# Kernel optimization log

Measured on AMD Instinct MI355X. Metric: run time of the kernel, lower is better.

The kernel has to match this reference:

```python
import jax, jax.numpy as jnp
import numpy as np

B, F, D, H = 16384, 10, 512, 8
DH = D // H
EPS = 1e-5


def setup_inputs() -> dict:
    key = jax.random.key(0)
    ks = jax.random.split(key, 12)
    s = 1.0 / np.sqrt(D)
    inp = {
        "x": jax.random.normal(ks[0], (B, F), dtype=jnp.float32),
        # per-feature Linear(1, D): weight (F, D), bias (F, D)
        "Wf": jax.random.normal(ks[1], (F, D), dtype=jnp.float32) * 1.0,
        "bf": jax.random.normal(ks[2], (F, D), dtype=jnp.float32) * 0.1,
        # MHA in/out projections (torch layout: out_features x in_features)
        "Wq": jax.random.normal(ks[3], (D, D), dtype=jnp.float32) * s,
        "Wk": jax.random.normal(ks[4], (D, D), dtype=jnp.float32) * s,
        "Wv": jax.random.normal(ks[5], (D, D), dtype=jnp.float32) * s,
        "bq": jax.random.normal(ks[6], (D,), dtype=jnp.float32) * 0.02,
        "bk": jax.random.normal(ks[7], (D,), dtype=jnp.float32) * 0.02,
        "bv": jax.random.normal(ks[8], (D,), dtype=jnp.float32) * 0.02,
        "Wo": jax.random.normal(ks[9], (D, D), dtype=jnp.float32) * s,
        "bo": jax.random.normal(ks[10], (D,), dtype=jnp.float32) * 0.02,
        "gamma": jnp.ones((D,), dtype=jnp.float32),
        "beta": jnp.zeros((D,), dtype=jnp.float32),
    }
    return inp


def reference(x, Wf, bf, Wq, Wk, Wv, bq, bk, bv, Wo, bo, gamma, beta):
    # Fused per-feature scalar Linear + ReLU: (B,F,1)*(F,D) + (F,D) -> (B,F,D)
    p = jax.nn.relu(x[:, :, None] * Wf[None] + bf[None])
    # Multi-head self-attention (q = k = v = p), torch Linear: y = x @ W.T + b
    def heads(t):  # (B,F,D) -> (B,H,F,DH)
        return t.reshape(B, F, H, DH).transpose(0, 2, 1, 3)
    q = heads(p @ Wq.T + bq)
    k = heads(p @ Wk.T + bk)
    v = heads(p @ Wv.T + bv)
    scores = jnp.einsum("bhqd,bhkd->bhqk", q, k) / jnp.sqrt(jnp.float32(DH))
    attn = jax.nn.softmax(scores, axis=-1)
    o = jnp.einsum("bhqk,bhkd->bhqd", attn, v)
    o = o.transpose(0, 2, 1, 3).reshape(B, F, D) @ Wo.T + bo
    # LayerNorm over last dim
    mu = jnp.mean(o, axis=-1, keepdims=True)
    var = jnp.mean(jnp.square(o - mu), axis=-1, keepdims=True)
    ln = (o - mu) * jax.lax.rsqrt(var + EPS) * gamma + beta
    # sum pool over the function/sequence axis
    return jnp.sum(ln, axis=1)  # (B, D)
```

## Files before the change

### kernel.cpp

```cpp
#include <hip/hip_runtime.h>
#include <stdint.h>


typedef __bf16 bf16;
typedef __bf16 bf16x8 __attribute__((ext_vector_type(8)));
typedef float f32x4 __attribute__((ext_vector_type(4)));

#define EPS 1e-5f

static constexpr size_t O_ELEMS   = (size_t)16384 * 10 * 512;
static constexpr size_t O_BYTES   = O_ELEMS * 2;
static constexpr size_t WQKV_ELEMS = (size_t)8 * 192 * 512;
static constexpr size_t WQKV_BYTES = WQKV_ELEMS * 2;

__device__ __forceinline__ void async_copy16(void* lds, const void* g) {
  __builtin_amdgcn_global_load_lds(
      (const __attribute__((address_space(1))) uint32_t*)g,
      (__attribute__((address_space(3))) uint32_t*)lds, 16, 0, 0);
}

__global__ __launch_bounds__(256) void pack_weights(
    const float* __restrict__ Wq, const float* __restrict__ Wk,
    const float* __restrict__ Wv, const float* __restrict__ Wo,
    bf16* __restrict__ wqkv, bf16* __restrict__ wob) {
  int idx = blockIdx.x * 256 + threadIdx.x;
#pragma unroll
  for (int u = 0; u < 4; ++u) {
    int i = idx + u * 262144;
    if (i < 786432) {
      int pr = i >> 9, k = i & 511;
      int h = pr / 192, w = pr - h * 192;
      int t = w >> 6, r = w & 63;
      const float* src = (t == 0) ? Wq : ((t == 1) ? Wk : Wv);
      wqkv[i] = (bf16)src[(h * 64 + r) * 512 + k];
    } else {
      int j = i - 786432;
      wob[j] = (bf16)Wo[j];
    }
  }
}

__global__ __launch_bounds__(512, 2) void kern_attn(
    const float* __restrict__ x, const float* __restrict__ Wf,
    const float* __restrict__ bfv, const bf16* __restrict__ wqkv,
    const float* __restrict__ bq, const float* __restrict__ bk,
    const float* __restrict__ bv, bf16* __restrict__ O) {
  __shared__ __align__(16) char sA[8 * 80 * 128];
  __shared__ __align__(16) char sB0[24576];
  __shared__ __align__(16) char sB1[24576];
  __shared__ __align__(16) char sQK[88 * 256];

  bf16* vbuf = (bf16*)sB1;
  float* scp = (float*)(sB1 + 10240);

  const int tid = threadIdx.x;
  const int wave = tid >> 6;
  const int lane = tid & 63;
  const int lm = lane & 15;
  const int lg = lane >> 4;
  const int wm = wave >> 2;
  const int wn = wave & 3;
  const int b0 = blockIdx.x * 8;
  const int lr = lane >> 3;
  const int kcp2 = lane & 7;
  const int kcg = kcp2 ^ lr;

#pragma unroll
  for (int jb = 0; jb < 3; ++jb) {
    int rb = wave + 8 * jb;
    async_copy16(sB0 + rb * 1024, wqkv + (size_t)(rb * 8 + lr) * 512 + kcg * 8);
  }

#pragma unroll
  for (int it = 0; it < 10; ++it) {
    int c = tid + it * 512;
    int s = c / 640, rem = c - s * 640;
    int r = rem >> 3, kcp = rem & 7;
    int kc = kcp ^ (r & 7);
    int k = s * 64 + kc * 8;
    int bl = r / 10, f = r - bl * 10;
    float xv = x[(b0 + bl) * 10 + f];
    const float* wf = Wf + f * 512 + k;
    const float* bp = bfv + f * 512 + k;
    bf16x8 pv;
#pragma unroll
    for (int j = 0; j < 8; ++j) pv[j] = (bf16)fmaxf(xv * wf[j] + bp[j], 0.f);
    *(bf16x8*)(sA + s * 10240 + r * 128 + kcp * 16) = pv;
  }
  __syncthreads();

  const int x7 = lm & 7;

  for (int h = 0; h < 8; ++h) {
    f32x4 acc[3][3];
#pragma unroll
    for (int i = 0; i < 3; ++i)
#pragma unroll
      for (int j = 0; j < 3; ++j) { f32x4 z = {0.f, 0.f, 0.f, 0.f}; acc[i][j] = z; }

    for (int s = 0; s < 8; ++s) {
      int t = h * 8 + s;
      char* bufC = (s & 1) ? sB1 : sB0;
      char* bufN = (s & 1) ? sB0 : sB1;
      if (t != 63) {
        int tn = t + 1;
        int h2 = tn >> 3, s2 = tn & 7;
        const bf16* srcb = wqkv + (size_t)h2 * 98304 + s2 * 64 + kcg * 8;
#pragma unroll
        for (int jb = 0; jb < 3; ++jb) {
          int rb = wave + 8 * jb;
          async_copy16(bufN + rb * 1024, srcb + (size_t)(rb * 8 + lr) * 512);
        }
      }
#pragma unroll
      for (int kk = 0; kk < 2; ++kk) {
        int kcl = kk * 4 + lg;
        int ch = (kcl ^ x7) << 4;
        bf16x8 af[3], bfr[3];
#pragma unroll
        for (int mt = 0; mt < 3; ++mt) {
          int m = wm * 48 + mt * 16 + lm;
          af[mt] = *(const bf16x8*)(sA + s * 10240 + m * 128 + ch);
        }
#pragma unroll
        for (int nt = 0; nt < 3; ++nt) {
          int n = wn * 48 + nt * 16 + lm;
          bfr[nt] = *(const bf16x8*)(bufC + n * 128 + ch);
        }
#pragma unroll
        for (int mt = 0; mt < 3; ++mt)
#pragma unroll
          for (int nt = 0; nt < 3; ++nt)
            acc[mt][nt] = __builtin_amdgcn_mfma_f32_16x16x32_bf16(af[mt], bfr[nt], acc[mt][nt], 0, 0, 0);
      }
      __syncthreads();
    }

    {
      float bias[3];
#pragma unroll
      for (int nt = 0; nt < 3; ++nt) {
        int col = wn * 48 + nt * 16 + lm;
        bias[nt] = (col < 64) ? bq[h * 64 + col]
                 : (col < 128) ? bk[h * 64 + col - 64]
                 : bv[h * 64 + col - 128];
      }
#pragma unroll
      for (int mt = 0; mt < 3; ++mt) {
        int rowb = wm * 48 + mt * 16 + lg * 4;
        if (rowb < 80) {
#pragma unroll
          for (int r = 0; r < 4; ++r) {
            int rw = rowb + r;
#pragma unroll
            for (int nt = 0; nt < 3; ++nt) {
              int col = wn * 48 + nt * 16 + lm;
              float val = acc[mt][nt][r] + bias[nt];
              if (col < 128)
                *(bf16*)(sQK + rw * 256 + (((col >> 3) ^ (rw & 7)) << 4) + (col & 7) * 2) = (bf16)val;
              else
                vbuf[rw * 64 + (col - 128)] = (bf16)val;
            }
          }
        }
      }
    }
    __syncthreads();

    {
      const int b = wave;
      f32x4 sv = {0.f, 0.f, 0.f, 0.f};
      const int rowa = b * 10 + lm;
      const int x7r = rowa & 7;
#pragma unroll
      for (int kk = 0; kk < 2; ++kk) {
        bf16x8 qf = *(const bf16x8*)(sQK + rowa * 256 + (((kk * 4 + lg) ^ x7r) << 4));
        bf16x8 kf = *(const bf16x8*)(sQK + rowa * 256 + (((8 + kk * 4 + lg) ^ x7r) << 4));
        sv = __builtin_amdgcn_mfma_f32_16x16x32_bf16(qf, kf, sv, 0, 0, 0);
      }
#pragma unroll
      for (int r = 0; r < 4; ++r) {
        float val = (lm < 10) ? sv[r] * 0.125f : -1e30f;
        float mx = val;
#pragma unroll
        for (int off = 1; off < 16; off <<= 1) mx = fmaxf(mx, __shfl_xor(mx, off));
        float e = __expf(val - mx);
        float ssum = e;
#pragma unroll
        for (int off = 1; off < 16; off <<= 1) ssum += __shfl_xor(ssum, off);
        int i = lg * 4 + r;
        if (i < 10 && lm < 12) scp[(b * 10 + i) * 12 + lm] = e / ssum;
      }
    }

    {
      const int b = wave;
      const int d = lane;
      float vv[10];
#pragma unroll
      for (int j = 0; j < 10; ++j) vv[j] = (float)vbuf[(b * 10 + j) * 64 + d];
      bf16* Ob = O + ((size_t)(b0 + b) * 10) * 512 + h * 64 + d;
#pragma unroll
      for (int i = 0; i < 10; ++i) {
        const float* ar = scp + (b * 10 + i) * 12;
        f32x4 a0 = *(const f32x4*)ar;
        f32x4 a1 = *(const f32x4*)(ar + 4);
        float o = a0[0] * vv[0] + a0[1] * vv[1] + a0[2] * vv[2] + a0[3] * vv[3]
                + a1[0] * vv[4] + a1[1] * vv[5] + a1[2] * vv[6] + a1[3] * vv[7]
                + ar[8] * vv[8] + ar[9] * vv[9];
        Ob[(size_t)i * 512] = (bf16)o;
      }
    }
    __syncthreads();
  }
}

__global__ __launch_bounds__(256, 2) void kern_out(
    const bf16* __restrict__ O, const bf16* __restrict__ wob,
    const float* __restrict__ bo, const float* __restrict__ gamma,
    const float* __restrict__ beta, float* __restrict__ out) {
  __shared__ __align__(16) char sAB[71680];
  __shared__ float partial[48][4][2];
  __shared__ float stats[48][2];
  char* As = sAB;
  char* Bs = sAB + 6144;
  bf16* lnb = (bf16*)sAB;

  const int tid = threadIdx.x;
  const int wave = tid >> 6, lane = tid & 63;
  const int lm = lane & 15, lg = lane >> 4;
  const int m0 = blockIdx.x * 40;

  f32x4 acc[3][8];
#pragma unroll
  for (int i = 0; i < 3; ++i)
#pragma unroll
    for (int j = 0; j < 8; ++j) { f32x4 z = {0.f, 0.f, 0.f, 0.f}; acc[i][j] = z; }

  const int lr = lane >> 3;
  const int kcp2 = lane & 7;
  const int kcg = kcp2 ^ lr;

  for (int s = 0; s < 8; ++s) {
    {
      int rr = wave * 8 + lr;
      int rm = min(rr, 39);
      async_copy16(As + wave * 1024, O + (size_t)(m0 + rm) * 512 + s * 64 + kcg * 8);
      if (wave < 2) {
        int rr2 = (4 + wave) * 8 + lr;
        int rm2 = min(rr2, 39);
        async_copy16(As + (4 + wave) * 1024, O + (size_t)(m0 + rm2) * 512 + s * 64 + kcg * 8);
      }
    }
#pragma unroll
    for (int jb = 0; jb < 16; ++jb) {
      int rb = wave + 4 * jb;
      int n = rb * 8 + lr;
      async_copy16(Bs + rb * 1024, wob + (size_t)n * 512 + s * 64 + kcg * 8);
    }
    __syncthreads();
#pragma unroll
    for (int kk = 0; kk < 2; ++kk) {
      int kcl = kk * 4 + lg;
      bf16x8 af[3], bfr[8];
#pragma unroll
      for (int mt = 0; mt < 3; ++mt) {
        int m = mt * 16 + lm;
        af[mt] = *(const bf16x8*)(As + m * 128 + ((kcl ^ (m & 7)) << 4));
      }
#pragma unroll
      for (int nt = 0; nt < 8; ++nt) {
        int n = wave * 128 + nt * 16 + lm;
        bfr[nt] = *(const bf16x8*)(Bs + n * 128 + ((kcl ^ (n & 7)) << 4));
      }
#pragma unroll
      for (int mt = 0; mt < 3; ++mt)
#pragma unroll
        for (int nt = 0; nt < 8; ++nt)
          acc[mt][nt] = __builtin_amdgcn_mfma_f32_16x16x32_bf16(af[mt], bfr[nt], acc[mt][nt], 0, 0, 0);
    }
    __syncthreads();
  }

#pragma unroll
  for (int nt = 0; nt < 8; ++nt) {
    int col = wave * 128 + nt * 16 + lm;
    float bb = bo[col];
#pragma unroll
    for (int mt = 0; mt < 3; ++mt)
#pragma unroll
      for (int r = 0; r < 4; ++r) acc[mt][nt][r] += bb;
  }

#pragma unroll
  for (int mt = 0; mt < 3; ++mt)
#pragma unroll
    for (int r = 0; r < 4; ++r) {
      float s1 = 0.f, s2 = 0.f;
#pragma unroll
      for (int nt = 0; nt < 8; ++nt) { float v = acc[mt][nt][r]; s1 += v; s2 += v * v; }
#pragma unroll
      for (int off = 1; off < 16; off <<= 1) {
        s1 += __shfl_xor(s1, off);
        s2 += __shfl_xor(s2, off);
      }
      if (lm == 0) {
        int row = mt * 16 + lg * 4 + r;
        partial[row][wave][0] = s1;
        partial[row][wave][1] = s2;
      }
    }
  __syncthreads();
  if (tid < 48) {
    float s1 = partial[tid][0][0] + partial[tid][1][0] + partial[tid][2][0] + partial[tid][3][0];
    float s2 = partial[tid][0][1] + partial[tid][1][1] + partial[tid][2][1] + partial[tid][3][1];
    float mu = s1 * (1.f / 512.f);
    float var = s2 * (1.f / 512.f) - mu * mu;
    stats[tid][0] = mu;
    stats[tid][1] = rsqrtf(var + EPS);
  }
  __syncthreads();
#pragma unroll
  for (int mt = 0; mt < 3; ++mt)
#pragma unroll
    for (int r = 0; r < 4; ++r) {
      int row = mt * 16 + lg * 4 + r;
      float mu = stats[row][0], rr = stats[row][1];
#pragma unroll
      for (int nt = 0; nt < 8; ++nt) {
        int col = wave * 128 + nt * 16 + lm;
        lnb[row * 520 + col] = (bf16)((acc[mt][nt][r] - mu) * rr);
      }
    }
  __syncthreads();
#pragma unroll
  for (int u = 0; u < 8; ++u) {
    int id = tid + u * 256;
    int b = id >> 9, n = id & 511;
    float ssum = 0.f;
#pragma unroll
    for (int f = 0; f < 10; ++f) ssum += (float)lnb[(b * 10 + f) * 520 + n];
    out[(size_t)(blockIdx.x * 4 + b) * 512 + n] = gamma[n] * ssum + 10.f * beta[n];
  }
}

extern "C" void kernel_launch(void* const* d_in, const int* in_sizes, int n_in,
                              void* d_out, int out_size, void* d_ws, size_t ws_size,
                              hipStream_t stream) {
  const float* x     = (const float*)d_in[0];
  const float* Wf    = (const float*)d_in[1];
  const float* bfv   = (const float*)d_in[2];
  const float* Wq    = (const float*)d_in[3];
  const float* Wk    = (const float*)d_in[4];
  const float* Wv    = (const float*)d_in[5];
  const float* bq    = (const float*)d_in[6];
  const float* bk    = (const float*)d_in[7];
  const float* bv    = (const float*)d_in[8];
  const float* Wo    = (const float*)d_in[9];
  const float* bo    = (const float*)d_in[10];
  const float* gamma = (const float*)d_in[11];
  const float* beta  = (const float*)d_in[12];
  float* out = (float*)d_out;

  char* ws = (char*)d_ws;
  bf16* O    = (bf16*)ws;
  bf16* wqkv = (bf16*)(ws + O_BYTES);
  bf16* wob  = (bf16*)(ws + O_BYTES + WQKV_BYTES);

  pack_weights<<<1024, 256, 0, stream>>>(Wq, Wk, Wv, Wo, wqkv, wob);
  kern_attn<<<2048, 512, 0, stream>>>(x, Wf, bfv, wqkv, bq, bk, bv, O);
  kern_out<<<4096, 256, 0, stream>>>(O, wob, bo, gamma, beta, out);
}
```

Baseline: 790.4 us.

## Fuse output projection and LayerNorm pooling into attention kernel

Merges the attention kernel and the output-projection/LayerNorm/sum-pool kernel into one launch, so each block processes its 80 rows through Wo right after computing attention. The O intermediate is still written to global memory, but it is read back by the same block, likely from L2, which avoids the separate launch and its 40-row tiling. The change also prefetches the A fragments for the next k-step into registers, skips the padded third m-tile for the upper waves, and raises MFMA wave priority with s_setprio. In exchange, LDS use grows to about 150KB per block, which may lower occupancy from the intended 2 blocks per CU.

```diff
diff --git a/kernel.cpp b/kernel.cpp
--- a/kernel.cpp
+++ b/kernel.cpp
@@ -10,8 +10,7 @@
 
 static constexpr size_t O_ELEMS   = (size_t)16384 * 10 * 512;
 static constexpr size_t O_BYTES   = O_ELEMS * 2;
-static constexpr size_t WQKV_ELEMS = (size_t)8 * 192 * 512;
-static constexpr size_t WQKV_BYTES = WQKV_ELEMS * 2;
+static constexpr size_t WQKV_BYTES = (size_t)8 * 192 * 512 * 2;
 
 __device__ __forceinline__ void async_copy16(void* lds, const void* g) {
   __builtin_amdgcn_global_load_lds(
@@ -40,16 +39,19 @@
   }
 }
 
-__global__ __launch_bounds__(512, 2) void kern_attn(
+__global__ __launch_bounds__(512, 2) void kern_fused(
     const float* __restrict__ x, const float* __restrict__ Wf,
     const float* __restrict__ bfv, const bf16* __restrict__ wqkv,
     const float* __restrict__ bq, const float* __restrict__ bk,
-    const float* __restrict__ bv, bf16* __restrict__ O) {
-  __shared__ __align__(16) char sA[8 * 80 * 128];
-  __shared__ __align__(16) char sB0[24576];
-  __shared__ __align__(16) char sB1[24576];
-  __shared__ __align__(16) char sQK[88 * 256];
-
+    const float* __restrict__ bv, bf16* __restrict__ O,
+    const bf16* __restrict__ wob, const float* __restrict__ bo,
+    const float* __restrict__ gamma, const float* __restrict__ beta,
+    float* __restrict__ out) {
+  __shared__ __align__(16) char smem[153600];
+  char* sA  = smem;
+  char* sB0 = smem + 81920;
+  char* sB1 = smem + 106496;
+  char* sQK = smem + 131072;
   bf16* vbuf = (bf16*)sB1;
   float* scp = (float*)(sB1 + 10240);
 
@@ -62,8 +64,8 @@
   const int wn = wave & 3;
   const int b0 = blockIdx.x * 8;
   const int lr = lane >> 3;
-  const int kcp2 = lane & 7;
-  const int kcg = kcp2 ^ lr;
+  const int kcg = (lane & 7) ^ lr;
+  const int x7 = lm & 7;
 
 #pragma unroll
   for (int jb = 0; jb < 3; ++jb) {
@@ -89,7 +91,15 @@
   }
   __syncthreads();
 
-  const int x7 = lm & 7;
+  bf16x8 af[2][3];
+#pragma unroll
+  for (int kk = 0; kk < 2; ++kk)
+#pragma unroll
+    for (int mt = 0; mt < 3; ++mt)
+      if (mt < 2 || wm == 0) {
+        int m = wm * 48 + mt * 16 + lm;
+        af[kk][mt] = *(const bf16x8*)(sA + m * 128 + (((kk * 4 + lg) ^ x7) << 4));
+      }
 
   for (int h = 0; h < 8; ++h) {
     f32x4 acc[3][3];
@@ -114,24 +124,32 @@
       }
 #pragma unroll
       for (int kk = 0; kk < 2; ++kk) {
-        int kcl = kk * 4 + lg;
-        int ch = (kcl ^ x7) << 4;
-        bf16x8 af[3], bfr[3];
-#pragma unroll
-        for (int mt = 0; mt < 3; ++mt) {
-          int m = wm * 48 + mt * 16 + lm;
-          af[mt] = *(const bf16x8*)(sA + s * 10240 + m * 128 + ch);
-        }
+        int ch = ((kk * 4 + lg) ^ x7) << 4;
+        bf16x8 bfr[3];
 #pragma unroll
         for (int nt = 0; nt < 3; ++nt) {
           int n = wn * 48 + nt * 16 + lm;
           bfr[nt] = *(const bf16x8*)(bufC + n * 128 + ch);
         }
+        __builtin_amdgcn_s_setprio(1);
 #pragma unroll
         for (int mt = 0; mt < 3; ++mt)
-#pragma unroll
-          for (int nt = 0; nt < 3; ++nt)
-            acc[mt][nt] = __builtin_amdgcn_mfma_f32_16x16x32_bf16(af[mt], bfr[nt], acc[mt][nt], 0, 0, 0);
+          if (mt < 2 || wm == 0)
+#pragma unroll
+            for (int nt = 0; nt < 3; ++nt)
+              acc[mt][nt] = __builtin_amdgcn_mfma_f32_16x16x32_bf16(af[kk][mt], bfr[nt], acc[mt][nt], 0, 0, 0);
+        __builtin_amdgcn_s_setprio(0);
+      }
+      {
+        const char* sAn = sA + ((s + 1) & 7) * 10240;
+#pragma unroll
+        for (int kk = 0; kk < 2; ++kk)
+#pragma unroll
+          for (int mt = 0; mt < 3; ++mt)
+            if (mt < 2 || wm == 0) {
+              int m = wm * 48 + mt * 16 + lm;
+              af[kk][mt] = *(const bf16x8*)(sAn + m * 128 + (((kk * 4 + lg) ^ x7) << 4));
+            }
       }
       __syncthreads();
     }
@@ -213,134 +231,123 @@
     }
     __syncthreads();
   }
-}
-
-__global__ __launch_bounds__(256, 2) void kern_out(
-    const bf16* __restrict__ O, const bf16* __restrict__ wob,
-    const float* __restrict__ bo, const float* __restrict__ gamma,
-    const float* __restrict__ beta, float* __restrict__ out) {
-  __shared__ __align__(16) char sAB[71680];
-  __shared__ float partial[48][4][2];
-  __shared__ float stats[48][2];
-  char* As = sAB;
-  char* Bs = sAB + 6144;
-  bf16* lnb = (bf16*)sAB;
-
-  const int tid = threadIdx.x;
-  const int wave = tid >> 6, lane = tid & 63;
-  const int lm = lane & 15, lg = lane >> 4;
-  const int m0 = blockIdx.x * 40;
-
-  f32x4 acc[3][8];
-#pragma unroll
-  for (int i = 0; i < 3; ++i)
-#pragma unroll
-    for (int j = 0; j < 8; ++j) { f32x4 z = {0.f, 0.f, 0.f, 0.f}; acc[i][j] = z; }
-
-  const int lr = lane >> 3;
-  const int kcp2 = lane & 7;
-  const int kcg = kcp2 ^ lr;
-
-  for (int s = 0; s < 8; ++s) {
-    {
-      int rr = wave * 8 + lr;
-      int rm = min(rr, 39);
-      async_copy16(As + wave * 1024, O + (size_t)(m0 + rm) * 512 + s * 64 + kcg * 8);
+
+  {
+    char* Ab = smem;
+    char* Bb = smem + 12288;
+    float* partial = (float*)(smem + 145920);
+    float* stats   = (float*)(smem + 148992);
+    const bf16* Osrc = O + (size_t)blockIdx.x * 80 * 512;
+
+    f32x4 acc[3][8];
+#pragma unroll
+    for (int i = 0; i < 3; ++i)
+#pragma unroll
+      for (int j = 0; j < 8; ++j) { f32x4 z = {0.f, 0.f, 0.f, 0.f}; acc[i][j] = z; }
+
+    for (int s = 0; s < 8; ++s) {
+      async_copy16(Ab + wave * 1024, Osrc + (size_t)(wave * 8 + lr) * 512 + s * 64 + kcg * 8);
       if (wave < 2) {
-        int rr2 = (4 + wave) * 8 + lr;
-        int rm2 = min(rr2, 39);
-        async_copy16(As + (4 + wave) * 1024, O + (size_t)(m0 + rm2) * 512 + s * 64 + kcg * 8);
-      }
-    }
-#pragma unroll
-    for (int jb = 0; jb < 16; ++jb) {
-      int rb = wave + 4 * jb;
-      int n = rb * 8 + lr;
-      async_copy16(Bs + rb * 1024, wob + (size_t)n * 512 + s * 64 + kcg * 8);
-    }
-    __syncthreads();
-#pragma unroll
-    for (int kk = 0; kk < 2; ++kk) {
-      int kcl = kk * 4 + lg;
-      bf16x8 af[3], bfr[8];
-#pragma unroll
-      for (int mt = 0; mt < 3; ++mt) {
-        int m = mt * 16 + lm;
-        af[mt] = *(const bf16x8*)(As + m * 128 + ((kcl ^ (m & 7)) << 4));
-      }
-#pragma unroll
-      for (int nt = 0; nt < 8; ++nt) {
-        int n = wave * 128 + nt * 16 + lm;
-        bfr[nt] = *(const bf16x8*)(Bs + n * 128 + ((kcl ^ (n & 7)) << 4));
-      }
+        int rb2 = 8 + wave;
+        async_copy16(Ab + rb2 * 1024, Osrc + (size_t)(rb2 * 8 + lr) * 512 + s * 64 + kcg * 8);
+      }
+#pragma unroll
+      for (int jb = 0; jb < 8; ++jb) {
+        int rb = wave + 8 * jb;
+        async_copy16(Bb + rb * 1024, wob + (size_t)(rb * 8 + lr) * 512 + s * 64 + kcg * 8);
+      }
+      __syncthreads();
+#pragma unroll
+      for (int kk = 0; kk < 2; ++kk) {
+        int ch = ((kk * 4 + lg) ^ x7) << 4;
+        bf16x8 a2[3], b2[8];
+#pragma unroll
+        for (int mt = 0; mt < 3; ++mt)
+          if (mt < 2 || wm == 0)
+            a2[mt] = *(const bf16x8*)(Ab + (wm * 48 + mt * 16 + lm) * 128 + ch);
+#pragma unroll
+        for (int nt = 0; nt < 8; ++nt)
+          b2[nt] = *(const bf16x8*)(Bb + (wn * 128 + nt * 16 + lm) * 128 + ch);
+        __builtin_amdgcn_s_setprio(1);
+#pragma unroll
+        for (int mt = 0; mt < 3; ++mt)
+          if (mt < 2 || wm == 0)
+#pragma unroll
+            for (int nt = 0; nt < 8; ++nt)
+              acc[mt][nt] = __builtin_amdgcn_mfma_f32_16x16x32_bf16(a2[mt], b2[nt], acc[mt][nt], 0, 0, 0);
+        __builtin_amdgcn_s_setprio(0);
+      }
+      __syncthreads();
+    }
+
+#pragma unroll
+    for (int nt = 0; nt < 8; ++nt) {
+      float bb = bo[wn * 128 + nt * 16 + lm];
 #pragma unroll
       for (int mt = 0; mt < 3; ++mt)
 #pragma unroll
-        for (int nt = 0; nt < 8; ++nt)
-          acc[mt][nt] = __builtin_amdgcn_mfma_f32_16x16x32_bf16(af[mt], bfr[nt], acc[mt][nt], 0, 0, 0);
-    }
-    __syncthreads();
-  }
-
-#pragma unroll
-  for (int nt = 0; nt < 8; ++nt) {
-    int col = wave * 128 + nt * 16 + lm;
-    float bb = bo[col];
+        for (int r = 0; r < 4; ++r) acc[mt][nt][r] += bb;
+    }
+
 #pragma unroll
     for (int mt = 0; mt < 3; ++mt)
 #pragma unroll
-      for (int r = 0; r < 4; ++r) acc[mt][nt][r] += bb;
-  }
-
-#pragma unroll
-  for (int mt = 0; mt < 3; ++mt)
-#pragma unroll
-    for (int r = 0; r < 4; ++r) {
+      for (int r = 0; r < 4; ++r) {
+        float s1 = 0.f, s2 = 0.f;
+#pragma unroll
+        for (int nt = 0; nt < 8; ++nt) { float v = acc[mt][nt][r]; s1 += v; s2 += v * v; }
+#pragma unroll
+        for (int off = 1; off < 16; off <<= 1) {
+          s1 += __shfl_xor(s1, off);
+          s2 += __shfl_xor(s2, off);
+        }
+        if (lm == 0) {
+          int row = wm * 48 + mt * 16 + lg * 4 + r;
+          if (row < 80) {
+            partial[(row * 4 + wn) * 2]     = s1;
+            partial[(row * 4 + wn) * 2 + 1] = s2;
+          }
+        }
+      }
+    __syncthreads();
+    if (tid < 80) {
       float s1 = 0.f, s2 = 0.f;
 #pragma unroll
-      for (int nt = 0; nt < 8; ++nt) { float v = acc[mt][nt][r]; s1 += v; s2 += v * v; }
-#pragma unroll
-      for (int off = 1; off < 16; off <<= 1) {
-        s1 += __shfl_xor(s1, off);
-        s2 += __shfl_xor(s2, off);
-      }
-      if (lm == 0) {
-        int row = mt * 16 + lg * 4 + r;
-        partial[row][wave][0] = s1;
-        partial[row][wave][1] = s2;
-      }
-    }
-  __syncthreads();
-  if (tid < 48) {
-    float s1 = partial[tid][0][0] + partial[tid][1][0] + partial[tid][2][0] + partial[tid][3][0];
-    float s2 = partial[tid][0][1] + partial[tid][1][1] + partial[tid][2][1] + partial[tid][3][1];
-    float mu = s1 * (1.f / 512.f);
-    float var = s2 * (1.f / 512.f) - mu * mu;
-    stats[tid][0] = mu;
-    stats[tid][1] = rsqrtf(var + EPS);
-  }
-  __syncthreads();
-#pragma unroll
-  for (int mt = 0; mt < 3; ++mt)
-#pragma unroll
-    for (int r = 0; r < 4; ++r) {
-      int row = mt * 16 + lg * 4 + r;
-      float mu = stats[row][0], rr = stats[row][1];
-#pragma unroll
-      for (int nt = 0; nt < 8; ++nt) {
-        int col = wave * 128 + nt * 16 + lm;
-        lnb[row * 520 + col] = (bf16)((acc[mt][nt][r] - mu) * rr);
-      }
-    }
-  __syncthreads();
-#pragma unroll
-  for (int u = 0; u < 8; ++u) {
-    int id = tid + u * 256;
-    int b = id >> 9, n = id & 511;
-    float ssum = 0.f;
-#pragma unroll
-    for (int f = 0; f < 10; ++f) ssum += (float)lnb[(b * 10 + f) * 520 + n];
-    out[(size_t)(blockIdx.x * 4 + b) * 512 + n] = gamma[n] * ssum + 10.f * beta[n];
+      for (int w = 0; w < 4; ++w) {
+        s1 += partial[(tid * 4 + w) * 2];
+        s2 += partial[(tid * 4 + w) * 2 + 1];
+      }
+      float mu = s1 * (1.f / 512.f);
+      float var = s2 * (1.f / 512.f) - mu * mu;
+      stats[tid * 2]     = mu;
+      stats[tid * 2 + 1] = rsqrtf(var + EPS);
+    }
+    __syncthreads();
+    bf16* lnb = (bf16*)smem;
+#pragma unroll
+    for (int mt = 0; mt < 3; ++mt)
+#pragma unroll
+      for (int r = 0; r < 4; ++r) {
+        int row = wm * 48 + mt * 16 + lg * 4 + r;
+        if (row < 80) {
+          float mu = stats[row * 2], rr = stats[row * 2 + 1];
+#pragma unroll
+          for (int nt = 0; nt < 8; ++nt) {
+            int col = wn * 128 + nt * 16 + lm;
+            lnb[row * 520 + col] = (bf16)((acc[mt][nt][r] - mu) * rr);
+          }
+        }
+      }
+    __syncthreads();
+#pragma unroll
+    for (int u = 0; u < 8; ++u) {
+      int id = tid + u * 512;
+      int b = id >> 9, n = id & 511;
+      float ssum = 0.f;
+#pragma unroll
+      for (int f = 0; f < 10; ++f) ssum += (float)lnb[(b * 10 + f) * 520 + n];
+      out[((size_t)blockIdx.x * 8 + b) * 512 + n] = gamma[n] * ssum + 10.f * beta[n];
+    }
   }
 }
 
@@ -368,6 +375,6 @@
   bf16* wob  = (bf16*)(ws + O_BYTES + WQKV_BYTES);
 
   pack_weights<<<1024, 256, 0, stream>>>(Wq, Wk, Wv, Wo, wqkv, wob);
-  kern_attn<<<2048, 512, 0, stream>>>(x, Wf, bfv, wqkv, bq, bk, bv, O);
-  kern_out<<<4096, 256, 0, stream>>>(O, wob, bo, gamma, beta, out);
+  kern_fused<<<2048, 512, 0, stream>>>(x, Wf, bfv, wqkv, bq, bk, bv, O,
+                                       wob, bo, gamma, beta, out);
 }
```

After: 755.8 us. 1.05x faster.
